# Kernel tuning notes

Measured on AMD Instinct MI355X. Metric: run time of the kernel, lower is better.

## Reference

```python
import jax, jax.numpy as jnp
import numpy as np
import math

D_MODEL = 1024
N_HEADS = 16
BATCH = 2
SEQ = 2048

def setup_inputs() -> dict:
    key = jax.random.key(0)
    ks = jax.random.split(key, 5)
    d = D_MODEL
    lim_qkv = 1.0 / math.sqrt(d)
    x = jax.random.normal(ks[0], (BATCH, SEQ, d), dtype=jnp.float32)
    qkv_w = jax.random.uniform(ks[1], (3 * d, d), dtype=jnp.float32, minval=-lim_qkv, maxval=lim_qkv)
    qkv_b = jax.random.uniform(ks[2], (3 * d,), dtype=jnp.float32, minval=-lim_qkv, maxval=lim_qkv)
    out_w = jax.random.uniform(ks[3], (d, d), dtype=jnp.float32, minval=-lim_qkv, maxval=lim_qkv)
    out_b = jax.random.uniform(ks[4], (d,), dtype=jnp.float32, minval=-lim_qkv, maxval=lim_qkv)
    return {"x": x, "qkv_w": qkv_w, "qkv_b": qkv_b, "out_w": out_w, "out_b": out_b}

def reference(x, qkv_w, qkv_b, out_w, out_b):
    b, s, d = x.shape
    h = N_HEADS
    hd = d // h
    # note: original uses float division for scale: sqrt(in_features / n_heads)
    scale = math.sqrt(d / h)
    qkv = x @ qkv_w.T + qkv_b                      # [b, s, 3d]
    q, k, v = jnp.split(qkv, 3, axis=-1)           # each [b, s, d]
    def heads(t):
        return t.reshape(b, s, h, hd).transpose(0, 2, 1, 3)  # [b, h, s, hd]
    qh, kh, vh = heads(q), heads(k), heads(v)
    # faithful quirk: scores = k @ q^T (k as query, q as key)
    scores = jnp.einsum('bhid,bhjd->bhij', kh, qh) / scale   # [b, h, s, s]
    alpha = jax.nn.softmax(scores, axis=-1)
    attn = jnp.einsum('bhij,bhjd->bhid', alpha, vh)          # [b, h, s, hd]
    attn = attn.transpose(0, 2, 1, 3).reshape(b, s, d)       # [b, s, d]
    return attn @ out_w.T + out_b
```

## Files before the change

kernel.cpp:

```cpp
#include <hip/hip_runtime.h>
#include <hip/hip_fp16.h>

#define D_MODEL 1024
#define N_HEADS 16
#define HEAD_DIM 64
#define BATCH 2
#define SEQ 2048
#define ROWS (BATCH*SEQ)

#define K_SCALE 0.18033688011112042f

using h8v = __attribute__((ext_vector_type(8))) _Float16;
using h4v = __attribute__((ext_vector_type(4))) _Float16;
using g2v = __attribute__((ext_vector_type(2))) __fp16;
using f4v = __attribute__((ext_vector_type(4))) float;

__device__ __forceinline__ ushort f2h_u(float x) { return __half_as_ushort(__float2half(x)); }
__device__ __forceinline__ void splith(float x, ushort& h, ushort& l) {
    __half hh_ = __float2half(x);
    h = __half_as_ushort(hh_);
    l = f2h_u(x - __half2float(hh_));
}

__device__ __forceinline__ size_t fidx(int row, int k) {
    return ((size_t)((row >> 7) * 32 + (k >> 5)) << 12)
         + (size_t)(((row & 127) >> 4) << 9)
         + (size_t)(((row & 15) * 4 + ((k & 31) >> 3)) << 3) + (k & 7);
}

__device__ __forceinline__ void async_lds16(const ushort* g, ushort* l) {
    __builtin_amdgcn_global_load_lds(
        (const __attribute__((address_space(1))) unsigned int*)g,
        (__attribute__((address_space(3))) unsigned int*)l, 16, 0, 0);
}

__global__ __launch_bounds__(256)
void prep_kernel(const float* __restrict__ x, const float* __restrict__ qw,
                 const float* __restrict__ ow,
                 ushort* __restrict__ xh, ushort* __restrict__ qwh,
                 ushort* __restrict__ owh, ushort* __restrict__ owl)
{
    const int b = blockIdx.x, t = threadIdx.x;
    if (b < 4096) {
        const int i = b * 256 + t;
        const int row = i >> 8, k4 = (i & 255) * 4;
        const float4 v = ((const float4*)x)[i];
        ushort4 h;
        h.x = f2h_u(v.x); h.y = f2h_u(v.y); h.z = f2h_u(v.z); h.w = f2h_u(v.w);
        *(ushort4*)&xh[fidx(row, k4)] = h;
    } else if (b < 7168) {
        const int i = (b - 4096) * 256 + t;
        const int row = i >> 8, k4 = (i & 255) * 4;
        const float4 v = ((const float4*)qw)[i];
        ushort4 h;
        h.x = f2h_u(v.x); h.y = f2h_u(v.y); h.z = f2h_u(v.z); h.w = f2h_u(v.w);
        *(ushort4*)&qwh[fidx(row, k4)] = h;
    } else {
        const int i = (b - 7168) * 256 + t;
        const int row = i >> 8, k4 = (i & 255) * 4;
        const float4 v = ((const float4*)ow)[i];
        const size_t o = fidx(row, k4);
        ushort4 h, l;
        splith(v.x, h.x, l.x); splith(v.y, h.y, l.y);
        splith(v.z, h.z, l.z); splith(v.w, h.w, l.w);
        *(ushort4*)&owh[o] = h; *(ushort4*)&owl[o] = l;
    }
}

__global__ __launch_bounds__(256, 5)
void gemm_qkv(const ushort* __restrict__ Af, const ushort* __restrict__ Wf,
              const float* __restrict__ bias,
              ushort* __restrict__ Qh, ushort* __restrict__ Kh,
              ushort* __restrict__ Vt)
{
    __shared__ ushort sA[2][4096], sW[2][2048];
    const int t = threadIdx.x, lane = t & 63, wv = t >> 6;
    const int tx = lane & 15, g = lane >> 4;
    const int lin = blockIdx.x;
    const int xcd = lin & 7, r = lin >> 3;
    const int mb = xcd * 4 + (r & 3);
    const int nb = r >> 2;
    const int at0 = (wv >> 1) * 4, wt0 = (wv & 1) * 2;
    const int fo = (tx * 4 + g) * 8;
    const size_t wbase = ((size_t)(nb & 1)) << 11;

    f4v acc[8];
#pragma unroll
    for (int i = 0; i < 8; i++)
#pragma unroll
        for (int e = 0; e < 4; e++) acc[i][e] = 0.f;

    {
        const size_t ao = ((size_t)(mb * 32)) << 12;
        const size_t wo = (((size_t)((nb >> 1) * 32)) << 12) + wbase;
#pragma unroll
        for (int c = 0; c < 2; c++) {
            const int o = (t + c * 256) * 8;
            async_lds16(Af + ao + o, &sA[0][o]);
        }
        async_lds16(Wf + wo + t * 8, &sW[0][t * 8]);
    }

    for (int kt = 0; kt < 32; kt++) {
        const int p = kt & 1;
        __syncthreads();
        if (kt < 31) {
            const size_t ao = ((size_t)(mb * 32 + kt + 1)) << 12;
            const size_t wo = (((size_t)((nb >> 1) * 32 + kt + 1)) << 12) + wbase;
#pragma unroll
            for (int c = 0; c < 2; c++) {
                const int o = (t + c * 256) * 8;
                async_lds16(Af + ao + o, &sA[p ^ 1][o]);
            }
            async_lds16(Wf + wo + t * 8, &sW[p ^ 1][t * 8]);
        }
        h8v ah[4], wh[2];
#pragma unroll
        for (int i = 0; i < 4; i++)
            ah[i] = *(const h8v*)&sA[p][(at0 + i) * 512 + fo];
#pragma unroll
        for (int i = 0; i < 2; i++)
            wh[i] = *(const h8v*)&sW[p][(wt0 + i) * 512 + fo];
        if (nb < 32) {
#pragma unroll
            for (int wi = 0; wi < 2; wi++)
#pragma unroll
                for (int ai = 0; ai < 4; ai++)
                    acc[wi * 4 + ai] = __builtin_amdgcn_mfma_f32_16x16x32_f16(wh[wi], ah[ai], acc[wi * 4 + ai], 0, 0, 0);
        } else {
#pragma unroll
            for (int ai = 0; ai < 4; ai++)
#pragma unroll
                for (int wi = 0; wi < 2; wi++)
                    acc[ai * 2 + wi] = __builtin_amdgcn_mfma_f32_16x16x32_f16(ah[ai], wh[wi], acc[ai * 2 + wi], 0, 0, 0);
        }
    }

    if (nb < 32) {
        const int part = nb >> 4;
        ushort* dst = part ? Kh : Qh;
        const float scale = part ? K_SCALE : 1.0f;
#pragma unroll
        for (int wi = 0; wi < 2; wi++) {
            const int gf0 = nb * 64 + (wv & 1) * 32 + wi * 16 + g * 4;
            const float4 bv = *(const float4*)&bias[gf0];
            const int gfl = gf0 & 1023;
            const int hh = gfl >> 6;
            const int dd = gfl & 63;
#pragma unroll
            for (int ai = 0; ai < 4; ai++) {
                const int s = mb * 128 + (wv >> 1) * 64 + ai * 16 + tx;
                const int bb = s >> 11, srel = s & 2047;
                const size_t idx = (size_t)(bb * N_HEADS + hh) * 131072
                    + (size_t)(srel >> 4) * 1024 + (size_t)(dd >> 5) * 512
                    + ((srel & 15) * 4 + ((dd & 31) >> 3)) * 8 + (dd & 7);
                const f4v a = acc[wi * 4 + ai];
                ushort4 h4;
                h4.x = f2h_u((a[0] + bv.x) * scale);
                h4.y = f2h_u((a[1] + bv.y) * scale);
                h4.z = f2h_u((a[2] + bv.z) * scale);
                h4.w = f2h_u((a[3] + bv.w) * scale);
                *(ushort4*)&dst[idx] = h4;
            }
        }
    } else {
#pragma unroll
        for (int wi = 0; wi < 2; wi++) {
            const int gf = nb * 64 + (wv & 1) * 32 + wi * 16 + tx;
            const float bv = bias[gf];
            const int gfl = gf & 1023;
            const int hh = gfl >> 6;
            const int dl = gfl & 63;
#pragma unroll
            for (int ai = 0; ai < 4; ai++) {
                const int jt0 = mb * 128 + (wv >> 1) * 64 + ai * 16 + g * 4;
                const int bb = jt0 >> 11, jr = jt0 & 2047;
                const size_t idx = (size_t)(bb * N_HEADS + hh) * 131072
                    + (size_t)(jr >> 6) * 4096
                    + (size_t)((((jr >> 4) & 3) * 4) + (dl >> 4)) * 256
                    + (((jr >> 2) & 3) * 16 + (dl & 15)) * 4;
                const f4v a = acc[ai * 2 + wi];
                ushort4 h4;
                h4.x = f2h_u(a[0] + bv);
                h4.y = f2h_u(a[1] + bv);
                h4.z = f2h_u(a[2] + bv);
                h4.w = f2h_u(a[3] + bv);
                *(ushort4*)&Vt[idx] = h4;
            }
        }
    }
}

__global__ __launch_bounds__(512)
void attn_mfma(const ushort* __restrict__ Kf, const ushort* __restrict__ Qf,
               const ushort* __restrict__ Vf,
               ushort* __restrict__ Oh, ushort* __restrict__ Ol)
{
    __shared__ ushort lds[16384];
    ushort* R0 = lds;
    ushort* R1 = lds + 8192;

    const int t = threadIdx.x, lane = t & 63, wv = t >> 6;
    const int tx = lane & 15, g = lane >> 4;
    const int lin = blockIdx.x;
    const int xcd = lin & 7, ix = lin >> 3;
    const int bh = xcd * 4 + (ix >> 4);
    const int it = ix & 15;
    const int b = bh >> 4, h = bh & 15;
    const int i0 = it * 128;
    const size_t hb = (size_t)bh * 131072;

    {
        const size_t kb = hb + (size_t)it * 8192;
#pragma unroll
        for (int c = 0; c < 2; c++) {
            const int o = (t + c * 512) * 8;
            async_lds16(Kf + kb + o, R0 + o);
        }
        const int o = t * 8;
        async_lds16(Qf + hb + o, R1 + o);
        async_lds16(Vf + hb + o, R1 + 4096 + o);
    }
    __syncthreads();

    const int fo = (tx * 4 + g) * 8;
    h8v kf[2];
#pragma unroll
    for (int kk = 0; kk < 2; kk++)
        kf[kk] = *(const h8v*)&R0[(wv * 2 + kk) * 512 + fo];

    f4v O[4];
    float l_acc = 0.f;
#pragma unroll
    for (int ht = 0; ht < 4; ht++)
#pragma unroll
        for (int e = 0; e < 4; e++) O[ht][e] = 0.f;

    for (int jt = 0; jt < SEQ / 64; jt++) {
        ushort* buf = (jt & 1) ? R0 : R1;
        ushort* nxt = (jt & 1) ? R1 : R0;
        __syncthreads();
        if (jt < SEQ / 64 - 1) {
            const size_t off = hb + (size_t)(jt + 1) * 4096;
            const int o = t * 8;
            async_lds16(Qf + off + o, nxt + o);
            async_lds16(Vf + off + o, nxt + 4096 + o);
        }
        const ushort* sQ = buf;
        const ushort* sV = buf + 4096;

        f4v sc[4];
#pragma unroll
        for (int jn = 0; jn < 4; jn++)
#pragma unroll
            for (int e = 0; e < 4; e++) sc[jn][e] = 0.f;
#pragma unroll
        for (int kk = 0; kk < 2; kk++)
#pragma unroll
            for (int jn = 0; jn < 4; jn++) {
                const h8v qf = *(const h8v*)&sQ[(jn * 2 + kk) * 512 + fo];
                sc[jn] = __builtin_amdgcn_mfma_f32_16x16x32_f16(qf, kf[kk], sc[jn], 0, 0, 0);
            }

        h4v ph[4];
#pragma unroll
        for (int jn = 0; jn < 4; jn++) {
            const float p0 = __builtin_amdgcn_exp2f(sc[jn][0]);
            const float p1 = __builtin_amdgcn_exp2f(sc[jn][1]);
            const float p2 = __builtin_amdgcn_exp2f(sc[jn][2]);
            const float p3 = __builtin_amdgcn_exp2f(sc[jn][3]);
            l_acc += (p0 + p1) + (p2 + p3);
            const g2v plo = __builtin_amdgcn_cvt_pkrtz(p0, p1);
            const g2v phi = __builtin_amdgcn_cvt_pkrtz(p2, p3);
            h4v pv;
            pv[0] = (_Float16)plo[0]; pv[1] = (_Float16)plo[1];
            pv[2] = (_Float16)phi[0]; pv[3] = (_Float16)phi[1];
            ph[jn] = pv;
        }

#pragma unroll
        for (int jc = 0; jc < 4; jc++)
#pragma unroll
            for (int ht = 0; ht < 4; ht++) {
                const h4v vf = *(const h4v*)&sV[(jc * 4 + ht) * 256 + (g * 16 + tx) * 4];
                O[ht] = __builtin_amdgcn_mfma_f32_16x16x16f16(vf, ph[jc], O[ht], 0, 0, 0);
            }
    }

    {
        float l = l_acc;
        l += __shfl_xor(l, 16);
        l += __shfl_xor(l, 32);
        const float inv = 1.0f / l;
        const int row = b * SEQ + i0 + wv * 16 + tx;
#pragma unroll
        for (int ht = 0; ht < 4; ht++) {
            const int k0 = h * 64 + ht * 16 + g * 4;
            const size_t o = fidx(row, k0);
            ushort4 hv, lv;
            float v;
            v = O[ht][0] * inv; splith(v, hv.x, lv.x);
            v = O[ht][1] * inv; splith(v, hv.y, lv.y);
            v = O[ht][2] * inv; splith(v, hv.z, lv.z);
            v = O[ht][3] * inv; splith(v, hv.w, lv.w);
            *(ushort4*)&Oh[o] = hv;
            *(ushort4*)&Ol[o] = lv;
        }
    }
}

__global__ __launch_bounds__(256, 4)
void gemm_out(const ushort* __restrict__ Af, const ushort* __restrict__ Alf,
              const ushort* __restrict__ Wf, const ushort* __restrict__ Wlf,
              const float* __restrict__ bias, float* __restrict__ out)
{
    __shared__ ushort sA[2][4096], sW[2][4096];
    const int t = threadIdx.x, lane = t & 63, wv = t >> 6;
    const int tx = lane & 15, g = lane >> 4;
    const int lin = blockIdx.x;
    const int xcd = lin & 7, r = lin >> 3;
    const int nb = xcd * 2 + (r & 1);
    const int mb = r >> 1;
    const int at0 = (wv >> 1) * 2, wt0 = (wv & 1) * 2;
    const int fo = (tx * 4 + g) * 8;
    const size_t abase = ((size_t)(mb & 1)) << 11;
    const size_t wbase = ((size_t)(nb & 1)) << 11;

    f4v acc[4];
#pragma unroll
    for (int i = 0; i < 4; i++)
#pragma unroll
        for (int e = 0; e < 4; e++) acc[i][e] = 0.f;

    {
        const size_t ao = (((size_t)((mb >> 1) * 32)) << 12) + abase;
        const size_t wo = (((size_t)((nb >> 1) * 32)) << 12) + wbase;
        const int o = t * 8;
        async_lds16(Af + ao + o, &sA[0][o]);
        async_lds16(Alf + ao + o, &sA[0][2048 + o]);
        async_lds16(Wf + wo + o, &sW[0][o]);
        async_lds16(Wlf + wo + o, &sW[0][2048 + o]);
    }

    for (int kt = 0; kt < 32; kt++) {
        const int p = kt & 1;
        __syncthreads();
        if (kt < 31) {
            const size_t ao = (((size_t)((mb >> 1) * 32 + kt + 1)) << 12) + abase;
            const size_t wo = (((size_t)((nb >> 1) * 32 + kt + 1)) << 12) + wbase;
            const int o = t * 8;
            async_lds16(Af + ao + o, &sA[p ^ 1][o]);
            async_lds16(Alf + ao + o, &sA[p ^ 1][2048 + o]);
            async_lds16(Wf + wo + o, &sW[p ^ 1][o]);
            async_lds16(Wlf + wo + o, &sW[p ^ 1][2048 + o]);
        }
        h8v ah[2], al[2], wh[2], wl[2];
#pragma unroll
        for (int i = 0; i < 2; i++) {
            ah[i] = *(const h8v*)&sA[p][(at0 + i) * 512 + fo];
            al[i] = *(const h8v*)&sA[p][2048 + (at0 + i) * 512 + fo];
            wh[i] = *(const h8v*)&sW[p][(wt0 + i) * 512 + fo];
            wl[i] = *(const h8v*)&sW[p][2048 + (wt0 + i) * 512 + fo];
        }
#pragma unroll
        for (int wi = 0; wi < 2; wi++)
#pragma unroll
            for (int ai = 0; ai < 2; ai++) {
                acc[wi * 2 + ai] = __builtin_amdgcn_mfma_f32_16x16x32_f16(wh[wi], ah[ai], acc[wi * 2 + ai], 0, 0, 0);
                acc[wi * 2 + ai] = __builtin_amdgcn_mfma_f32_16x16x32_f16(wh[wi], al[ai], acc[wi * 2 + ai], 0, 0, 0);
                acc[wi * 2 + ai] = __builtin_amdgcn_mfma_f32_16x16x32_f16(wl[wi], ah[ai], acc[wi * 2 + ai], 0, 0, 0);
            }
    }

#pragma unroll
    for (int wi = 0; wi < 2; wi++) {
        const int gf0 = nb * 64 + (wv & 1) * 32 + wi * 16 + g * 4;
        const float4 bv = *(const float4*)&bias[gf0];
#pragma unroll
        for (int ai = 0; ai < 2; ai++) {
            const int tok = mb * 64 + (wv >> 1) * 32 + ai * 16 + tx;
            const f4v a = acc[wi * 2 + ai];
            float4 o;
            o.x = a[0] + bv.x;
            o.y = a[1] + bv.y;
            o.z = a[2] + bv.z;
            o.w = a[3] + bv.w;
            *(float4*)&out[(size_t)tok * D_MODEL + gf0] = o;
        }
    }
}

extern "C" void kernel_launch(void* const* d_in, const int* in_sizes, int n_in,
                              void* d_out, int out_size, void* d_ws, size_t ws_size,
                              hipStream_t stream) {
    const float* x     = (const float*)d_in[0];
    const float* qkv_w = (const float*)d_in[1];
    const float* qkv_b = (const float*)d_in[2];
    const float* out_w = (const float*)d_in[3];
    const float* out_b = (const float*)d_in[4];
    float* out = (float*)d_out;

    const size_t FB = (size_t)ROWS * D_MODEL;
    const size_t MM = (size_t)D_MODEL * D_MODEL;
    ushort* u   = (ushort*)d_ws;
    ushort* xh  = u;
    ushort* Ol  = u + FB;
    ushort* Qh  = u + 2 * FB;
    ushort* Kh  = u + 3 * FB;
    ushort* Vt  = u + 4 * FB;
    ushort* qwh = u + 5 * FB;
    ushort* owh = u + 5 * FB + 3 * MM;
    ushort* owl = owh + MM;

    prep_kernel<<<8192, 256, 0, stream>>>(x, qkv_w, out_w, xh, qwh, owh, owl);
    gemm_qkv<<<1536, 256, 0, stream>>>(xh, qwh, qkv_b, Qh, Kh, Vt);
    attn_mfma<<<512, 512, 0, stream>>>(Kh, Qh, Vt, xh, Ol);
    gemm_out<<<1024, 256, 0, stream>>>(xh, Ol, owh, owl, out_b, out);
}
```

Baseline: 211.7 us.

## Software-pipeline attention loop across three LDS buffers to overlap exp with MFMA

Restructures the attention inner loop so the QK^T MFMAs of tile j run alongside the PV MFMAs of tile j-1. The exp/convert work of the current tile is issued after the PV MFMAs instead of blocking them. K now stays in its own LDS region, and Q/V use a rotating triple buffer, which raises LDS use from 32KB to 64KB per block. The aim is to hide the transcendental latency and the dependency stalls between the two GEMMs, at the cost of more LDS and registers, which could lower occupancy. It also packs the half vectors with a shufflevector instead of per-element moves.

Result: faster. 204.9 us (-3.2%).

```diff
diff --git a/kernel.cpp b/kernel.cpp
--- a/kernel.cpp
+++ b/kernel.cpp
@@ -13,6 +13,7 @@
 using h8v = __attribute__((ext_vector_type(8))) _Float16;
 using h4v = __attribute__((ext_vector_type(4))) _Float16;
 using g2v = __attribute__((ext_vector_type(2))) __fp16;
+using g4v = __attribute__((ext_vector_type(4))) __fp16;
 using f4v = __attribute__((ext_vector_type(4))) float;
 
 __device__ __forceinline__ ushort f2h_u(float x) { return __half_as_ushort(__float2half(x)); }
@@ -196,9 +197,9 @@
                const ushort* __restrict__ Vf,
                ushort* __restrict__ Oh, ushort* __restrict__ Ol)
 {
-    __shared__ ushort lds[16384];
-    ushort* R0 = lds;
-    ushort* R1 = lds + 8192;
+    __shared__ ushort lds[32768];
+    ushort* KR = lds;
+    ushort* bufs = lds + 8192;
 
     const int t = threadIdx.x, lane = t & 63, wv = t >> 6;
     const int tx = lane & 15, g = lane >> 4;
@@ -215,11 +216,11 @@
 #pragma unroll
         for (int c = 0; c < 2; c++) {
             const int o = (t + c * 512) * 8;
-            async_lds16(Kf + kb + o, R0 + o);
+            async_lds16(Kf + kb + o, KR + o);
         }
         const int o = t * 8;
-        async_lds16(Qf + hb + o, R1 + o);
-        async_lds16(Vf + hb + o, R1 + 4096 + o);
+        async_lds16(Qf + hb + o, bufs + o);
+        async_lds16(Vf + hb + o, bufs + 4096 + o);
     }
     __syncthreads();
 
@@ -227,7 +228,14 @@
     h8v kf[2];
 #pragma unroll
     for (int kk = 0; kk < 2; kk++)
-        kf[kk] = *(const h8v*)&R0[(wv * 2 + kk) * 512 + fo];
+        kf[kk] = *(const h8v*)&KR[(wv * 2 + kk) * 512 + fo];
+
+    {
+        const size_t off = hb + 4096;
+        const int o = t * 8;
+        async_lds16(Qf + off + o, bufs + 8192 + o);
+        async_lds16(Vf + off + o, bufs + 8192 + 4096 + o);
+    }
 
     f4v O[4];
     float l_acc = 0.f;
@@ -236,19 +244,10 @@
 #pragma unroll
         for (int e = 0; e < 4; e++) O[ht][e] = 0.f;
 
-    for (int jt = 0; jt < SEQ / 64; jt++) {
-        ushort* buf = (jt & 1) ? R0 : R1;
-        ushort* nxt = (jt & 1) ? R1 : R0;
-        __syncthreads();
-        if (jt < SEQ / 64 - 1) {
-            const size_t off = hb + (size_t)(jt + 1) * 4096;
-            const int o = t * 8;
-            async_lds16(Qf + off + o, nxt + o);
-            async_lds16(Vf + off + o, nxt + 4096 + o);
-        }
-        const ushort* sQ = buf;
-        const ushort* sV = buf + 4096;
-
+    h4v php[4];
+
+    {
+        const ushort* sQ = bufs;
         f4v sc[4];
 #pragma unroll
         for (int jn = 0; jn < 4; jn++)
@@ -261,8 +260,6 @@
                 const h8v qf = *(const h8v*)&sQ[(jn * 2 + kk) * 512 + fo];
                 sc[jn] = __builtin_amdgcn_mfma_f32_16x16x32_f16(qf, kf[kk], sc[jn], 0, 0, 0);
             }
-
-        h4v ph[4];
 #pragma unroll
         for (int jn = 0; jn < 4; jn++) {
             const float p0 = __builtin_amdgcn_exp2f(sc[jn][0]);
@@ -272,18 +269,68 @@
             l_acc += (p0 + p1) + (p2 + p3);
             const g2v plo = __builtin_amdgcn_cvt_pkrtz(p0, p1);
             const g2v phi = __builtin_amdgcn_cvt_pkrtz(p2, p3);
-            h4v pv;
-            pv[0] = (_Float16)plo[0]; pv[1] = (_Float16)plo[1];
-            pv[2] = (_Float16)phi[0]; pv[3] = (_Float16)phi[1];
-            ph[jn] = pv;
-        }
+            const g4v pk = __builtin_shufflevector(plo, phi, 0, 1, 2, 3);
+            php[jn] = __builtin_bit_cast(h4v, pk);
+        }
+    }
+
+    int bp = 0, bc = 1, bn = 2;
+    for (int jt = 1; jt < SEQ / 64; jt++) {
+        __syncthreads();
+        if (jt < SEQ / 64 - 1) {
+            const size_t off = hb + (size_t)(jt + 1) * 4096;
+            const int o = t * 8;
+            async_lds16(Qf + off + o, bufs + bn * 8192 + o);
+            async_lds16(Vf + off + o, bufs + bn * 8192 + 4096 + o);
+        }
+        const ushort* sQ = bufs + bc * 8192;
+        const ushort* sVp = bufs + bp * 8192 + 4096;
+
+        f4v sc[4];
+#pragma unroll
+        for (int jn = 0; jn < 4; jn++)
+#pragma unroll
+            for (int e = 0; e < 4; e++) sc[jn][e] = 0.f;
+#pragma unroll
+        for (int kk = 0; kk < 2; kk++)
+#pragma unroll
+            for (int jn = 0; jn < 4; jn++) {
+                const h8v qf = *(const h8v*)&sQ[(jn * 2 + kk) * 512 + fo];
+                sc[jn] = __builtin_amdgcn_mfma_f32_16x16x32_f16(qf, kf[kk], sc[jn], 0, 0, 0);
+            }
 
 #pragma unroll
         for (int jc = 0; jc < 4; jc++)
 #pragma unroll
             for (int ht = 0; ht < 4; ht++) {
-                const h4v vf = *(const h4v*)&sV[(jc * 4 + ht) * 256 + (g * 16 + tx) * 4];
-                O[ht] = __builtin_amdgcn_mfma_f32_16x16x16f16(vf, ph[jc], O[ht], 0, 0, 0);
+                const h4v vf = *(const h4v*)&sVp[(jc * 4 + ht) * 256 + (g * 16 + tx) * 4];
+                O[ht] = __builtin_amdgcn_mfma_f32_16x16x16f16(vf, php[jc], O[ht], 0, 0, 0);
+            }
+
+#pragma unroll
+        for (int jn = 0; jn < 4; jn++) {
+            const float p0 = __builtin_amdgcn_exp2f(sc[jn][0]);
+            const float p1 = __builtin_amdgcn_exp2f(sc[jn][1]);
+            const float p2 = __builtin_amdgcn_exp2f(sc[jn][2]);
+            const float p3 = __builtin_amdgcn_exp2f(sc[jn][3]);
+            l_acc += (p0 + p1) + (p2 + p3);
+            const g2v plo = __builtin_amdgcn_cvt_pkrtz(p0, p1);
+            const g2v phi = __builtin_amdgcn_cvt_pkrtz(p2, p3);
+            const g4v pk = __builtin_shufflevector(plo, phi, 0, 1, 2, 3);
+            php[jn] = __builtin_bit_cast(h4v, pk);
+        }
+
+        const int tmp = bp; bp = bc; bc = bn; bn = tmp;
+    }
+
+    {
+        const ushort* sVp = bufs + bp * 8192 + 4096;
+#pragma unroll
+        for (int jc = 0; jc < 4; jc++)
+#pragma unroll
+            for (int ht = 0; ht < 4; ht++) {
+                const h4v vf = *(const h4v*)&sVp[(jc * 4 + ht) * 256 + (g * 16 + tx) * 4];
+                O[ht] = __builtin_amdgcn_mfma_f32_16x16x16f16(vf, php[jc], O[ht], 0, 0, 0);
             }
     }
 
```
